# Kernel tuning notes

Measured on AMD Instinct MI355X. Metric: run time of the kernel, lower is better.

The kernel has to match this reference:

```python
import jax, jax.numpy as jnp
import numpy as np

N_CLASSES = 4096
FEAT_DIM = 2048


def setup_inputs() -> dict:
    key = jax.random.key(0)
    k1, k2, k3 = jax.random.split(key, 3)
    boundaries = jax.random.uniform(k1, (N_CLASSES,), dtype=jnp.float32)
    prototypes = jax.random.normal(k2, (N_CLASSES, FEAT_DIM), dtype=jnp.float32)
    classifier_weights = jax.random.normal(k3, (N_CLASSES, FEAT_DIM), dtype=jnp.float32)
    return {"boundaries": boundaries, "prototypes": prototypes,
            "classifier_weights": classifier_weights}


def reference(boundaries, prototypes, classifier_weights):
    n = boundaries.shape[0]
    # L2-normalize prototypes along feature dim (F.normalize, eps=1e-12)
    norm = jnp.sqrt(jnp.sum(prototypes * prototypes, axis=-1, keepdims=True))
    p = prototypes / jnp.maximum(norm, 1e-12)
    # s[i, j] = <p_i, w_j>  -- one GEMM instead of N^2 tiny dots
    s = p @ classifier_weights.T  # [N, N]
    diag = jnp.diagonal(s)  # <p_i, w_i>, shape [N]
    # term1 depends only on i, term2 on (i, j)
    term1 = (1.0 - boundaries) * diag  # [N]
    term2 = s * (boundaries - 1.0)[None, :]  # [N, N], broadcast over j
    vals = jax.nn.relu(term1[:, None] + term2)  # [N, N]
    # exclude i == j
    off_diag_sum = jnp.sum(vals) - jnp.sum(jnp.diagonal(vals))
    return off_diag_sum / (n * (n - 1))
```

## Files before the change

kernel.cpp:

```cpp
#include <hip/hip_runtime.h>
#include <hip/hip_bf16.h>

#define N_CLS 4096
#define FDIM  2048
#define NT    16

typedef float  floatx4 __attribute__((ext_vector_type(4)));
typedef int    intx2   __attribute__((ext_vector_type(2)));
typedef int    intx4   __attribute__((ext_vector_type(4)));
typedef int    intx8   __attribute__((ext_vector_type(8)));

__global__ __launch_bounds__(256) void prep_kernel(
    const float* __restrict__ bnd,
    const float* __restrict__ proto,
    const float* __restrict__ wgt,
    unsigned char* __restrict__ pf8,
    unsigned char* __restrict__ wf8,
    float* __restrict__ t1,
    float* __restrict__ cc,
    float* __restrict__ accum)
{
    const int row = blockIdx.x;
    const int tid = threadIdx.x;
    const size_t base = (size_t)row * FDIM + (size_t)tid * 8;

    floatx4 p0 = *(const floatx4*)(proto + base);
    floatx4 p1 = *(const floatx4*)(proto + base + 4);
    floatx4 w0 = *(const floatx4*)(wgt + base);
    floatx4 w1 = *(const floatx4*)(wgt + base + 4);

    float ss = 0.f, dt = 0.f;
#pragma unroll
    for (int k = 0; k < 4; ++k) {
        ss += p0[k] * p0[k] + p1[k] * p1[k];
        dt += p0[k] * w0[k] + p1[k] * w1[k];
    }
#pragma unroll
    for (int off = 32; off > 0; off >>= 1) {
        ss += __shfl_down(ss, off);
        dt += __shfl_down(dt, off);
    }

    __shared__ float sss[4], sdt[4];
    __shared__ float srn;
    const int wid = tid >> 6, lane = tid & 63;
    if (lane == 0) { sss[wid] = ss; sdt[wid] = dt; }
    __syncthreads();
    if (tid == 0) {
        float SS = sss[0] + sss[1] + sss[2] + sss[3];
        float DT = sdt[0] + sdt[1] + sdt[2] + sdt[3];
        float rn = 1.0f / fmaxf(sqrtf(SS), 1e-12f);
        srn = rn;
        float bv = bnd[row];
        t1[row] = (1.0f - bv) * (DT * rn);
        cc[row] = bv - 1.0f;
        if (row == 0) *accum = 0.0f;
    }
    __syncthreads();
    const float rn = srn;

    intx2 pv, wv;
    {
        int a = __builtin_amdgcn_cvt_pk_fp8_f32(p0[0] * rn, p0[1] * rn, 0, 0);
        a     = __builtin_amdgcn_cvt_pk_fp8_f32(p0[2] * rn, p0[3] * rn, a, 1);
        int b = __builtin_amdgcn_cvt_pk_fp8_f32(p1[0] * rn, p1[1] * rn, 0, 0);
        b     = __builtin_amdgcn_cvt_pk_fp8_f32(p1[2] * rn, p1[3] * rn, b, 1);
        pv[0] = a; pv[1] = b;
        int c = __builtin_amdgcn_cvt_pk_fp8_f32(w0[0], w0[1], 0, 0);
        c     = __builtin_amdgcn_cvt_pk_fp8_f32(w0[2], w0[3], c, 1);
        int d = __builtin_amdgcn_cvt_pk_fp8_f32(w1[0], w1[1], 0, 0);
        d     = __builtin_amdgcn_cvt_pk_fp8_f32(w1[2], w1[3], d, 1);
        wv[0] = c; wv[1] = d;
    }
    *(intx2*)(pf8 + base) = pv;
    *(intx2*)(wf8 + base) = wv;
}

__global__ __launch_bounds__(256, 2) void gemm_reduce_kernel(
    const unsigned char* __restrict__ A,
    const unsigned char* __restrict__ B,
    const float* __restrict__ t1,
    const float* __restrict__ cc,
    float* __restrict__ accum)
{
    __shared__ unsigned char sAB[2][32768];
    __shared__ float red[4];

    const int tid  = threadIdx.x;
    const int wid  = tid >> 6;
    const int lane = tid & 63;
    const int SC1  = 0x7F7F7F7F;

    const int b   = blockIdx.x;
    const int xcd = b & 7, sl = b >> 3;
    const int bi  = ((xcd & 1) << 4) | (sl & 15);
    const int bj  = ((xcd >> 1) << 3) | (sl >> 4);
    const int arow0 = bi * 128;
    const int brow0 = bj * 128;

    const int wm = wid >> 1;
    const int wn = wid & 1;
    const int lr = lane & 15;
    const int q  = lane >> 4;
    const int r7 = lane & 7;

    const int cq0 = ((2 * q)     ^ r7) << 4;
    const int cq1 = ((2 * q + 1) ^ r7) << 4;
    const int aoff = (wm * 64 + lr) * 128;
    const int boff = 16384 + (wn * 64 + lr) * 128;

    const int srow = tid >> 3;
    const int sgc  = ((tid & 7) ^ ((tid >> 3) & 7)) << 4;

    auto glds = [&](const unsigned char* src, unsigned char* dst) {
        __builtin_amdgcn_global_load_lds(
            (const __attribute__((address_space(1))) void*)src,
            (__attribute__((address_space(3))) void*)dst, 16, 0, 0);
    };
    auto stageA = [&](int t, int bn) {
#pragma unroll
        for (int c = 0; c < 4; ++c)
            glds(A + (size_t)(arow0 + c * 32 + srow) * FDIM + t * 128 + sgc,
                 &sAB[bn][c * 4096 + tid * 16]);
    };
    auto stageB = [&](int t, int bn) {
#pragma unroll
        for (int c = 0; c < 4; ++c)
            glds(B + (size_t)(brow0 + c * 32 + srow) * FDIM + t * 128 + sgc,
                 &sAB[bn][16384 + c * 4096 + tid * 16]);
    };

    floatx4 acc[4][4];
#pragma unroll
    for (int m = 0; m < 4; ++m)
#pragma unroll
        for (int n = 0; n < 4; ++n) acc[m][n] = (floatx4)0.0f;

    stageA(0, 0); stageB(0, 0);
    __syncthreads();

    int buf = 0;
#pragma unroll 1
    for (int t = 0; t < NT; ++t) {
        if (t + 1 < NT) { stageA(t + 1, buf ^ 1); stageB(t + 1, buf ^ 1); }

        intx8 fa[4], fb[4];
#pragma unroll
        for (int mi = 0; mi < 4; ++mi) {
            const unsigned char* bp = &sAB[buf][aoff + mi * 2048];
            intx4 lo = *(const intx4*)(bp + cq0);
            intx4 hi = *(const intx4*)(bp + cq1);
            fa[mi] = __builtin_shufflevector(lo, hi, 0, 1, 2, 3, 4, 5, 6, 7);
        }
#pragma unroll
        for (int ni = 0; ni < 4; ++ni) {
            const unsigned char* bp = &sAB[buf][boff + ni * 2048];
            intx4 lo = *(const intx4*)(bp + cq0);
            intx4 hi = *(const intx4*)(bp + cq1);
            fb[ni] = __builtin_shufflevector(lo, hi, 0, 1, 2, 3, 4, 5, 6, 7);
        }
#pragma unroll
        for (int mi = 0; mi < 4; ++mi)
#pragma unroll
            for (int ni = 0; ni < 4; ++ni)
                acc[mi][ni] = __builtin_amdgcn_mfma_scale_f32_16x16x128_f8f6f4(
                    fa[mi], fb[ni], acc[mi][ni], 0, 0, 0, SC1, 0, SC1);

        __syncthreads();
        buf ^= 1;
    }

    const int row0 = arow0 + wm * 64 + (lane >> 4) * 4;
    const int col0 = brow0 + wn * 64 + lr;

    float local = 0.f;
#pragma unroll
    for (int n = 0; n < 4; ++n) {
        const int j = col0 + n * 16;
        const float cj = cc[j];
#pragma unroll
        for (int m = 0; m < 4; ++m) {
#pragma unroll
            for (int r = 0; r < 4; ++r) {
                const int i = row0 + m * 16 + r;
                float v = fmaxf(t1[i] + acc[m][n][r] * cj, 0.f);
                local += (i == j) ? 0.f : v;
            }
        }
    }

#pragma unroll
    for (int off = 32; off > 0; off >>= 1)
        local += __shfl_down(local, off);
    if (lane == 0) red[wid] = local;
    __syncthreads();
    if (tid == 0)
        atomicAdd(accum, red[0] + red[1] + red[2] + red[3]);
}

__global__ void finalize_kernel(const float* __restrict__ accum,
                                float* __restrict__ out)
{
    const float denom = 4096.0f * 4095.0f;
    out[0] = *accum / denom;
}

extern "C" void kernel_launch(void* const* d_in, const int* in_sizes, int n_in,
                              void* d_out, int out_size, void* d_ws, size_t ws_size,
                              hipStream_t stream) {
    const float* bnd   = (const float*)d_in[0];
    const float* proto = (const float*)d_in[1];
    const float* wgt   = (const float*)d_in[2];

    char* ws = (char*)d_ws;
    unsigned char* pf8 = (unsigned char*)ws;
    unsigned char* wf8 = (unsigned char*)(ws + (size_t)N_CLS * FDIM);
    float* t1    = (float*)(ws + (size_t)N_CLS * FDIM * 2);
    float* cc    = t1 + N_CLS;
    float* accum = cc + N_CLS;

    prep_kernel<<<N_CLS, 256, 0, stream>>>(bnd, proto, wgt, pf8, wf8, t1, cc, accum);
    gemm_reduce_kernel<<<1024, 256, 0, stream>>>(pf8, wf8, t1, cc, accum);
    finalize_kernel<<<1, 1, 0, stream>>>(accum, (float*)d_out);
}
```

Before: 64.62 us.

## Interleave GEMM tile staging with MFMA quadrants using phased barriers

Restructures the FP8 GEMM main loop into four phases. Each phase waits on a partial vmcnt, takes a lightweight barrier, reads half of the A/B fragments from LDS, issues one pair of next-tile global-to-LDS loads, and runs a 2x2 quadrant of MFMAs raised to higher priority. This replaces the old pattern of issuing all next-tile loads at once followed by a single full sync. The LDS chunk swizzle is also permuted consistently for both operands, changing the K-chunk layout and read addresses. The aim is to overlap global loads, LDS reads and matrix math more finely. The cost is more barriers, hand-tuned waitcnt values that must exactly match the number of outstanding loads, and a redundant dummy load in the final iteration.

```diff
diff --git a/kernel.cpp b/kernel.cpp
--- a/kernel.cpp
+++ b/kernel.cpp
@@ -76,6 +76,33 @@
     *(intx2*)(wf8 + base) = wv;
 }
 
+#define PH_BAR() { __builtin_amdgcn_s_barrier(); __builtin_amdgcn_sched_barrier(0); }
+#define VMCNT(N) asm volatile("s_waitcnt vmcnt(" #N ")" ::: "memory")
+
+#define RD_FA2(D, MI0)                                                         \
+    _Pragma("unroll") for (int k = 0; k < 2; ++k) {                            \
+        const unsigned char* bp = &sAB[D][aoff + ((MI0) + k) * 2048];          \
+        intx4* fp = (intx4*)&fa[(MI0) + k];                                    \
+        fp[0] = *(const intx4*)(bp + cq0);                                     \
+        fp[1] = *(const intx4*)(bp + cq1);                                     \
+    }
+#define RD_FB2(D, NI0)                                                         \
+    _Pragma("unroll") for (int k = 0; k < 2; ++k) {                            \
+        const unsigned char* bp = &sAB[D][boff + ((NI0) + k) * 2048];          \
+        intx4* fp = (intx4*)&fb[(NI0) + k];                                    \
+        fp[0] = *(const intx4*)(bp + cq0);                                     \
+        fp[1] = *(const intx4*)(bp + cq1);                                     \
+    }
+#define MFMA_Q2(MI0, NI0)                                                      \
+    __builtin_amdgcn_s_setprio(1);                                             \
+    _Pragma("unroll") for (int mi = 0; mi < 2; ++mi)                           \
+    _Pragma("unroll") for (int ni = 0; ni < 2; ++ni)                           \
+        acc[(MI0)+mi][(NI0)+ni] =                                              \
+            __builtin_amdgcn_mfma_scale_f32_16x16x128_f8f6f4(                  \
+                fa[(MI0)+mi], fb[(NI0)+ni], acc[(MI0)+mi][(NI0)+ni],           \
+                0, 0, 0, SC1, 0, SC1);                                         \
+    __builtin_amdgcn_s_setprio(0);
+
 __global__ __launch_bounds__(256, 2) void gemm_reduce_kernel(
     const unsigned char* __restrict__ A,
     const unsigned char* __restrict__ B,
@@ -104,30 +131,35 @@
     const int q  = lane >> 4;
     const int r7 = lane & 7;
 
-    const int cq0 = ((2 * q)     ^ r7) << 4;
-    const int cq1 = ((2 * q + 1) ^ r7) << 4;
+    const int cq0 = ((q)     ^ r7) << 4;
+    const int cq1 = ((4 | q) ^ r7) << 4;
     const int aoff = (wm * 64 + lr) * 128;
     const int boff = 16384 + (wn * 64 + lr) * 128;
 
     const int srow = tid >> 3;
-    const int sgc  = ((tid & 7) ^ ((tid >> 3) & 7)) << 4;
+    const int sx   = (tid & 7) ^ ((tid >> 3) & 7);
+    const int sgc  = (((sx & 3) << 1) | (sx >> 2)) << 4;
 
     auto glds = [&](const unsigned char* src, unsigned char* dst) {
         __builtin_amdgcn_global_load_lds(
             (const __attribute__((address_space(1))) void*)src,
             (__attribute__((address_space(3))) void*)dst, 16, 0, 0);
     };
-    auto stageA = [&](int t, int bn) {
-#pragma unroll
-        for (int c = 0; c < 4; ++c)
+    auto stageApair = [&](int pair, int t) {
+#pragma unroll
+        for (int h = 0; h < 2; ++h) {
+            const int c = pair + 2 * h;
             glds(A + (size_t)(arow0 + c * 32 + srow) * FDIM + t * 128 + sgc,
-                 &sAB[bn][c * 4096 + tid * 16]);
+                 &sAB[t & 1][c * 4096 + tid * 16]);
+        }
     };
-    auto stageB = [&](int t, int bn) {
-#pragma unroll
-        for (int c = 0; c < 4; ++c)
+    auto stageBpair = [&](int pair, int t) {
+#pragma unroll
+        for (int h = 0; h < 2; ++h) {
+            const int c = pair + 2 * h;
             glds(B + (size_t)(brow0 + c * 32 + srow) * FDIM + t * 128 + sgc,
-                 &sAB[bn][16384 + c * 4096 + tid * 16]);
+                 &sAB[t & 1][16384 + c * 4096 + tid * 16]);
+        }
     };
 
     floatx4 acc[4][4];
@@ -136,38 +168,34 @@
 #pragma unroll
         for (int n = 0; n < 4; ++n) acc[m][n] = (floatx4)0.0f;
 
-    stageA(0, 0); stageB(0, 0);
-    __syncthreads();
-
-    int buf = 0;
+    intx8 fa[4];
+    intx8 fb[4];
+
+    stageApair(0, 0); stageBpair(0, 0); stageBpair(1, 0); stageApair(1, 0);
+
 #pragma unroll 1
     for (int t = 0; t < NT; ++t) {
-        if (t + 1 < NT) { stageA(t + 1, buf ^ 1); stageB(t + 1, buf ^ 1); }
-
-        intx8 fa[4], fb[4];
-#pragma unroll
-        for (int mi = 0; mi < 4; ++mi) {
-            const unsigned char* bp = &sAB[buf][aoff + mi * 2048];
-            intx4 lo = *(const intx4*)(bp + cq0);
-            intx4 hi = *(const intx4*)(bp + cq1);
-            fa[mi] = __builtin_shufflevector(lo, hi, 0, 1, 2, 3, 4, 5, 6, 7);
-        }
-#pragma unroll
-        for (int ni = 0; ni < 4; ++ni) {
-            const unsigned char* bp = &sAB[buf][boff + ni * 2048];
-            intx4 lo = *(const intx4*)(bp + cq0);
-            intx4 hi = *(const intx4*)(bp + cq1);
-            fb[ni] = __builtin_shufflevector(lo, hi, 0, 1, 2, 3, 4, 5, 6, 7);
-        }
-#pragma unroll
-        for (int mi = 0; mi < 4; ++mi)
-#pragma unroll
-            for (int ni = 0; ni < 4; ++ni)
-                acc[mi][ni] = __builtin_amdgcn_mfma_scale_f32_16x16x128_f8f6f4(
-                    fa[mi], fb[ni], acc[mi][ni], 0, 0, 0, SC1, 0, SC1);
-
-        __syncthreads();
-        buf ^= 1;
+        const int D  = t & 1;
+        const int tn = (t + 1 > NT - 1) ? NT - 2 : t + 1;
+
+        VMCNT(4);
+        PH_BAR();
+        RD_FA2(D, 0); RD_FB2(D, 0);
+        stageApair(0, tn);
+        MFMA_Q2(0, 0);
+        VMCNT(4);
+        PH_BAR();
+        RD_FB2(D, 2);
+        stageBpair(0, tn);
+        MFMA_Q2(0, 2);
+        VMCNT(4);
+        PH_BAR();
+        RD_FA2(D, 2);
+        stageBpair(1, tn);
+        MFMA_Q2(2, 2);
+        PH_BAR();
+        stageApair(1, tn);
+        MFMA_Q2(2, 0);
     }
 
     const int row0 = arow0 + wm * 64 + (lane >> 4) * 4;
```

New measurement: 63.59 us. Within noise of the previous version (-1.6%).
